# Kernel optimization log

Measured on AMD Instinct MI355X. Metric: run time of the kernel, lower is better.

Reference implementation:

```python
import jax, jax.numpy as jnp
import numpy as np

P = 2.0
HARDNESS_RATIO = 0.1
MARGIN = 0.0
EPS = 1e-7

N, DFEAT, NCLS = 4096, 128, 64


def setup_inputs() -> dict:
    key = jax.random.key(0)
    kx, ky = jax.random.split(key)
    x = jax.random.normal(kx, (N, DFEAT), dtype=jnp.float32)
    y = jax.random.randint(ky, (N,), 0, NCLS, dtype=jnp.int64)
    return {"x": x, "y": y}


def reference(x, y):
    # torch.cdist(x, x, p=2) via gram-matrix identity (clamped for sqrt stability)
    sq = jnp.sum(x * x, axis=1)                      # [N]
    D2 = sq[:, None] + sq[None, :] - 2.0 * (x @ x.T)  # [N, N]
    D = jnp.sqrt(jnp.maximum(D2, 1e-12))

    # label agreement masks (no-grad in torch; integer-derived so no float grad anyway)
    agree = (y[None, :] == y[:, None]).astype(x.dtype)   # [N, N]
    disagree = 1.0 - agree
    # With 64 samples/class every row is valid (>=1 positive and >=1 negative),
    # so the torch valid_rows filter keeps all rows; we compute all rows.

    # sort each row by distance, drop self (column 0), gather
    col_idx = jnp.argsort(D, axis=1)[:, 1:]               # [N, N-1]
    dist = jnp.take_along_axis(D, col_idx, axis=1)        # [N, N-1]
    a = jnp.take_along_axis(agree, col_idx, axis=1)
    d = jnp.take_along_axis(disagree, col_idx, axis=1)

    found_agree = jnp.cumsum(a, axis=1)
    found_agree = found_agree / (jnp.sum(found_agree, axis=1, keepdims=True) + EPS)
    found_disagree = jnp.cumsum(d, axis=1)
    found_disagree = found_disagree / (jnp.sum(found_disagree, axis=1, keepdims=True) + EPS)

    negative_hardness = jax.lax.stop_gradient(d * (found_disagree / (found_agree + HARDNESS_RATIO)))
    positive_hardness = jax.lax.stop_gradient(a * ((found_disagree + HARDNESS_RATIO) / (found_agree + HARDNESS_RATIO)))

    per_sample_score = jnp.mean(
        jax.nn.relu(dist * positive_hardness + MARGIN - dist * negative_hardness), axis=1
    )  # [N]

    sample_performance = jnp.sum(found_agree - found_disagree, axis=1)
    sample_performance = sample_performance - jnp.min(sample_performance)
    sample_weight = jax.lax.stop_gradient(1.0 / (sample_performance + 1.0))
    return per_sample_score * sample_weight
```

## Files before the change

kernel.cpp:

```cpp
#include <hip/hip_runtime.h>
#include <math.h>
#include <float.h>


#define N 4096
#define DF 128
#define NCLS 64
#define MAXP 128
#define DSTR 128
#define NB 256
#define HPAD 260
#define BSCALE 0.5f

typedef __bf16 bf16x8 __attribute__((ext_vector_type(8)));
typedef float f32x4 __attribute__((ext_vector_type(4)));
typedef unsigned int u32x4 __attribute__((ext_vector_type(4)));

static __device__ __forceinline__ unsigned short f2bf(float f) {
  unsigned int u = __float_as_uint(f);
  unsigned int r = (u + 0x7fffu + ((u >> 16) & 1u)) >> 16;
  return (unsigned short)r;
}
static __device__ __forceinline__ int d2bin(float d2) {
  int b = (int)(d2 * BSCALE);
  return min(max(b, 0), NB - 1);
}

__global__ void k_prep(const float* __restrict__ x, const int* __restrict__ y,
                       unsigned short* __restrict__ xb, float* __restrict__ sq,
                       unsigned int* __restrict__ cls_cnt, int* __restrict__ cls_idx,
                       int* __restrict__ pos, unsigned int* __restrict__ hist) {
  __shared__ unsigned int c_cnt[NCLS];
  const int tid = threadIdx.x;
  if (blockIdx.x < 1024) {
    const int wave = tid >> 6, lane = tid & 63;
    const int row = (blockIdx.x << 2) + wave;
    const float2 v = *(const float2*)&x[row * DF + (lane << 1)];
    unsigned int b = (unsigned int)f2bf(v.x) | ((unsigned int)f2bf(v.y) << 16);
    *(unsigned int*)&xb[row * DF + (lane << 1)] = b;
    const u32x4 z = {0u, 0u, 0u, 0u};
    *(u32x4*)&hist[(size_t)blockIdx.x * 1024 + (tid << 2)] = z;
    float s = v.x * v.x + v.y * v.y;
    #pragma unroll
    for (int off = 32; off; off >>= 1) s += __shfl_down(s, off);
    if (lane == 0) sq[row] = s;
  } else {
    if (tid < NCLS) c_cnt[tid] = 0u;
    __syncthreads();
    for (int k = tid; k < N; k += 256) {
      const int c = y[k];
      unsigned int p = atomicAdd(&c_cnt[c], 1u);
      if (p >= MAXP) p = MAXP - 1;
      cls_idx[c * MAXP + p] = k;
      pos[k] = (int)p;
    }
    __syncthreads();
    if (tid < NCLS) cls_cnt[tid] = min(c_cnt[tid], (unsigned int)MAXP);
  }
}

__global__ __launch_bounds__(256) void k_gram(
    const unsigned short* __restrict__ xb, const float* __restrict__ sq,
    const unsigned int* __restrict__ cls_cnt, const int* __restrict__ cls_idx,
    float* __restrict__ d2f) {
  __shared__ int plist[MAXP];
  __shared__ float sqL[MAXP];
  const int c = blockIdx.x >> 3;
  const int ti = blockIdx.x & 7;
  const int M = (int)cls_cnt[c];
  const int nT = (M + 15) >> 4;
  if (ti >= nT) return;
  const int tid = threadIdx.x;
  for (int m = tid; m < M; m += 256) {
    const int j = cls_idx[c * MAXP + m];
    plist[m] = j;
    sqL[m] = sq[j];
  }
  __syncthreads();
  const int wave = tid >> 6, lane = tid & 63;
  const int l15 = lane & 15, lg = lane >> 4;
  const int ra = min(ti * 16 + l15, M - 1);
  const u32x4* ap = (const u32x4*)(xb + (size_t)plist[ra] * DF + (lg << 3));
  const bf16x8 a0 = __builtin_bit_cast(bf16x8, ap[0]);
  const bf16x8 a1 = __builtin_bit_cast(bf16x8, ap[4]);
  const bf16x8 a2 = __builtin_bit_cast(bf16x8, ap[8]);
  const bf16x8 a3 = __builtin_bit_cast(bf16x8, ap[12]);
  float sqa[4];
  #pragma unroll
  for (int r = 0; r < 4; ++r) sqa[r] = sqL[min(ti * 16 + lg * 4 + r, M - 1)];
  float* drow = d2f + (size_t)c * (MAXP * DSTR);
  for (int tj = wave; tj < nT; tj += 4) {
    const int rb = min(tj * 16 + l15, M - 1);
    const u32x4* bp = (const u32x4*)(xb + (size_t)plist[rb] * DF + (lg << 3));
    const bf16x8 b0 = __builtin_bit_cast(bf16x8, bp[0]);
    const bf16x8 b1 = __builtin_bit_cast(bf16x8, bp[4]);
    const bf16x8 b2 = __builtin_bit_cast(bf16x8, bp[8]);
    const bf16x8 b3 = __builtin_bit_cast(bf16x8, bp[12]);
    f32x4 acc = {0.f, 0.f, 0.f, 0.f};
    acc = __builtin_amdgcn_mfma_f32_16x16x32_bf16(a0, b0, acc, 0, 0, 0);
    acc = __builtin_amdgcn_mfma_f32_16x16x32_bf16(a1, b1, acc, 0, 0, 0);
    acc = __builtin_amdgcn_mfma_f32_16x16x32_bf16(a2, b2, acc, 0, 0, 0);
    acc = __builtin_amdgcn_mfma_f32_16x16x32_bf16(a3, b3, acc, 0, 0, 0);
    const float sqc = sqL[rb];
    #pragma unroll
    for (int r = 0; r < 4; ++r) {
      const int row = ti * 16 + lg * 4 + r;
      drow[row * DSTR + tj * 16 + l15] = fmaf(-2.0f, acc[r], sqa[r] + sqc);
    }
  }
}

#define ROWS 32
#define CS 8

__global__ __launch_bounds__(256, 4) void k_count(
    const unsigned short* __restrict__ xb, const float* __restrict__ sq,
    unsigned int* __restrict__ hist) {
  __shared__ unsigned int histL[ROWS][HPAD];
  __shared__ float sqcL[512];
  const int rb = blockIdx.x >> 3;
  const int cs = blockIdx.x & 7;
  const int row0 = rb * ROWS;
  const int col0 = cs * 512;
  const int tid = threadIdx.x;
  const int wave = tid >> 6, lane = tid & 63;
  const int l15 = lane & 15, lg = lane >> 4;

  for (int e = tid; e < ROWS * HPAD; e += 256) ((unsigned int*)histL)[e] = 0u;
  if (tid < 256) { sqcL[tid] = sq[col0 + tid]; sqcL[tid + 256] = sq[col0 + 256 + tid]; }

  const u32x4* apA = (const u32x4*)(xb + (size_t)(row0 + l15) * DF + (lg << 3));
  const u32x4* apB = (const u32x4*)(xb + (size_t)(row0 + 16 + l15) * DF + (lg << 3));
  const bf16x8 a0 = __builtin_bit_cast(bf16x8, apA[0]);
  const bf16x8 a1 = __builtin_bit_cast(bf16x8, apA[4]);
  const bf16x8 a2 = __builtin_bit_cast(bf16x8, apA[8]);
  const bf16x8 a3 = __builtin_bit_cast(bf16x8, apA[12]);
  const bf16x8 a4 = __builtin_bit_cast(bf16x8, apB[0]);
  const bf16x8 a5 = __builtin_bit_cast(bf16x8, apB[4]);
  const bf16x8 a6 = __builtin_bit_cast(bf16x8, apB[8]);
  const bf16x8 a7 = __builtin_bit_cast(bf16x8, apB[12]);
  float sqa0[4], sqa1[4];
  #pragma unroll
  for (int r = 0; r < 4; ++r) {
    sqa0[r] = sq[row0 + lg * 4 + r];
    sqa1[r] = sq[row0 + 16 + lg * 4 + r];
  }
  __syncthreads();

  const int jbase = wave * 128;
  #pragma unroll
  for (int t = 0; t < 8; ++t) {
    const int jc = jbase + t * 16;
    const u32x4* bp = (const u32x4*)(xb + (size_t)(col0 + jc + l15) * DF + (lg << 3));
    const bf16x8 b0 = __builtin_bit_cast(bf16x8, bp[0]);
    const bf16x8 b1 = __builtin_bit_cast(bf16x8, bp[4]);
    const bf16x8 b2 = __builtin_bit_cast(bf16x8, bp[8]);
    const bf16x8 b3 = __builtin_bit_cast(bf16x8, bp[12]);
    f32x4 acc0 = {0.f, 0.f, 0.f, 0.f};
    f32x4 acc1 = {0.f, 0.f, 0.f, 0.f};
    acc0 = __builtin_amdgcn_mfma_f32_16x16x32_bf16(a0, b0, acc0, 0, 0, 0);
    acc0 = __builtin_amdgcn_mfma_f32_16x16x32_bf16(a1, b1, acc0, 0, 0, 0);
    acc0 = __builtin_amdgcn_mfma_f32_16x16x32_bf16(a2, b2, acc0, 0, 0, 0);
    acc0 = __builtin_amdgcn_mfma_f32_16x16x32_bf16(a3, b3, acc0, 0, 0, 0);
    acc1 = __builtin_amdgcn_mfma_f32_16x16x32_bf16(a4, b0, acc1, 0, 0, 0);
    acc1 = __builtin_amdgcn_mfma_f32_16x16x32_bf16(a5, b1, acc1, 0, 0, 0);
    acc1 = __builtin_amdgcn_mfma_f32_16x16x32_bf16(a6, b2, acc1, 0, 0, 0);
    acc1 = __builtin_amdgcn_mfma_f32_16x16x32_bf16(a7, b3, acc1, 0, 0, 0);
    const float sqc = sqcL[jc + l15];
    #pragma unroll
    for (int r = 0; r < 4; ++r) {
      const int lr = lg * 4 + r;
      atomicAdd(&histL[lr][d2bin(fmaf(-2.0f, acc0[r], sqa0[r] + sqc))], 1u);
      atomicAdd(&histL[16 + lr][d2bin(fmaf(-2.0f, acc1[r], sqa1[r] + sqc))], 1u);
    }
  }
  __syncthreads();
  for (int e = tid; e < ROWS * NB; e += 256) {
    const unsigned int v = histL[e >> 8][e & 255];
    if (v) atomicAdd(&hist[(size_t)(row0 + (e >> 8)) * NB + (e & 255)], v);
  }
}

__global__ void k_final(const int* __restrict__ y, const int* __restrict__ pos,
                        const unsigned int* __restrict__ cls_cnt,
                        const float* __restrict__ d2f,
                        const unsigned int* __restrict__ hist,
                        float* __restrict__ out) {
  __shared__ float rowL[MAXP];
  __shared__ unsigned int preL[NB];
  const int i = blockIdx.x;
  const int lane = threadIdx.x;
  const int c = y[i];
  const int rw = pos[i];
  const int M = (int)cls_cnt[c];
  const float* drow = d2f + (size_t)c * (MAXP * DSTR) + (size_t)rw * DSTR;
  rowL[lane] = drow[lane];
  rowL[lane + 64] = drow[lane + 64];
  const u32x4 h = *(const u32x4*)&hist[(size_t)i * NB + (lane << 2)];
  const unsigned int s0 = h[0], s1 = s0 + h[1], s2 = s1 + h[2], s3 = s2 + h[3];
  unsigned int sc_ = s3;
  #pragma unroll
  for (int off = 1; off < 64; off <<= 1) {
    const unsigned int t = __shfl_up(sc_, off);
    if (lane >= off) sc_ += t;
  }
  const unsigned int base = sc_ - s3;
  preL[(lane << 2) + 0] = base + s0;
  preL[(lane << 2) + 1] = base + s1;
  preL[(lane << 2) + 2] = base + s2;
  preL[(lane << 2) + 3] = base + s3;
  __syncthreads();
  const float dself = rowL[rw];
  const int el0 = lane, el1 = lane + 64;
  const bool v0 = (el0 < M) && (el0 != rw);
  const bool v1 = (el1 < M) && (el1 != rw);
  const float dt0 = v0 ? rowL[el0] : 0.f;
  const float dt1 = v1 ? rowL[el1] : 0.f;
  int r0 = 0, r1 = 0;
  for (int s = 0; s < M; ++s) {
    const float ds = rowL[s];
    r0 += (ds < dt0 || (ds == dt0 && s < el0)) ? 1 : 0;
    r1 += (ds < dt1 || (ds == dt1 && s < el1)) ? 1 : 0;
  }
  r0 -= (dself < dt0 || (dself == dt0 && rw < el0)) ? 1 : 0;
  r1 -= (dself < dt1 || (dself == dt1 && rw < el1)) ? 1 : 0;
  const int pr0 = v0 ? (int)preL[d2bin(dt0)] : 0;
  const int pr1 = v1 ? (int)preL[d2bin(dt1)] : 0;
  int sa = 0;
  if (v0) sa += (N + 1) - pr0;
  if (v1) sa += (N + 1) - pr1;
  #pragma unroll
  for (int off = 32; off; off >>= 1) sa += __shfl_down(sa, off);
  sa = __shfl(sa, 0);
  const float Sa = (float)sa + 1e-7f;
  const float Sd = (float)(8386560 - sa) + 1e-7f;
  float sc = 0.f;
  if (v0) {
    const float fa = (float)(r0 + 1) / Sa;
    const float fd = (float)((pr0 - 1) - (r0 + 1)) / Sd;
    sc += sqrtf(fmaxf(dt0, 1e-12f)) * (fd + 0.1f) / (fa + 0.1f);
  }
  if (v1) {
    const float fa = (float)(r1 + 1) / Sa;
    const float fd = (float)((pr1 - 1) - (r1 + 1)) / Sd;
    sc += sqrtf(fmaxf(dt1, 1e-12f)) * (fd + 0.1f) / (fa + 0.1f);
  }
  #pragma unroll
  for (int off = 32; off; off >>= 1) sc += __shfl_down(sc, off);
  if (lane == 0) out[i] = sc * (1.0f / 4095.0f);
}

extern "C" void kernel_launch(void* const* d_in, const int* in_sizes, int n_in,
                              void* d_out, int out_size, void* d_ws, size_t ws_size,
                              hipStream_t stream) {
  const float* x = (const float*)d_in[0];
  const int* y = (const int*)d_in[1];
  float* out = (float*)d_out;
  char* ws = (char*)d_ws;
  unsigned short* xb    = (unsigned short*)ws;
  float* sq             = (float*)(ws + 1048576);
  unsigned int* cls_cnt = (unsigned int*)(ws + 1064960);
  int* cls_idx          = (int*)(ws + 1065216);
  int* pos              = (int*)(ws + 1097984);
  unsigned int* hist    = (unsigned int*)(ws + 1114368);
  float* d2f            = (float*)(ws + 5308672);

  k_prep<<<1025, 256, 0, stream>>>(x, y, xb, sq, cls_cnt, cls_idx, pos, hist);
  k_gram<<<NCLS * 8, 256, 0, stream>>>(xb, sq, cls_cnt, cls_idx, d2f);
  k_count<<<(N / ROWS) * CS, 256, 0, stream>>>(xb, sq, hist);
  k_final<<<N, 64, 0, stream>>>(y, pos, cls_cnt, d2f, hist, out);
}
```

Measured before the change: 104.7 us.

## Fuse gram and count kernels; write per-slice histograms instead of global atomics

Merges the in-class gram kernel and the histogram-count kernel into a single launch, with block ranges dispatching to each role. It also replaces global atomic accumulation of histograms with plain stores of per-column-slice partial histograms, which the final kernel sums, so the zeroing pass in the prep kernel goes away. The count tiles are reshaped to 16 rows by 1024 columns and the LDS histogram padding changes. The intent is to cut one launch, the global atomics and the zero-fill, at the cost of more histogram memory traffic and less A-fragment reuse per B load.

```diff
diff --git a/kernel.cpp b/kernel.cpp
--- a/kernel.cpp
+++ b/kernel.cpp
@@ -9,8 +9,12 @@
 #define MAXP 128
 #define DSTR 128
 #define NB 256
-#define HPAD 260
+#define ROWS 16
+#define CS 4
+#define HPAD 257
+#define HROW (CS * NB)
 #define BSCALE 0.5f
+#define KCNT ((N / ROWS) * CS)
 
 typedef __bf16 bf16x8 __attribute__((ext_vector_type(8)));
 typedef float f32x4 __attribute__((ext_vector_type(4)));
@@ -29,7 +33,7 @@
 __global__ void k_prep(const float* __restrict__ x, const int* __restrict__ y,
                        unsigned short* __restrict__ xb, float* __restrict__ sq,
                        unsigned int* __restrict__ cls_cnt, int* __restrict__ cls_idx,
-                       int* __restrict__ pos, unsigned int* __restrict__ hist) {
+                       int* __restrict__ pos) {
   __shared__ unsigned int c_cnt[NCLS];
   const int tid = threadIdx.x;
   if (blockIdx.x < 1024) {
@@ -38,8 +42,6 @@
     const float2 v = *(const float2*)&x[row * DF + (lane << 1)];
     unsigned int b = (unsigned int)f2bf(v.x) | ((unsigned int)f2bf(v.y) << 16);
     *(unsigned int*)&xb[row * DF + (lane << 1)] = b;
-    const u32x4 z = {0u, 0u, 0u, 0u};
-    *(u32x4*)&hist[(size_t)blockIdx.x * 1024 + (tid << 2)] = z;
     float s = v.x * v.x + v.y * v.y;
     #pragma unroll
     for (int off = 32; off; off >>= 1) s += __shfl_down(s, off);
@@ -59,132 +61,110 @@
   }
 }
 
-__global__ __launch_bounds__(256) void k_gram(
+__global__ __launch_bounds__(256, 4) void k_cg(
     const unsigned short* __restrict__ xb, const float* __restrict__ sq,
     const unsigned int* __restrict__ cls_cnt, const int* __restrict__ cls_idx,
-    float* __restrict__ d2f) {
+    unsigned int* __restrict__ hist4, float* __restrict__ d2f) {
+  __shared__ unsigned int histL[ROWS][HPAD];
+  __shared__ float sqcL[1024];
   __shared__ int plist[MAXP];
   __shared__ float sqL[MAXP];
-  const int c = blockIdx.x >> 3;
-  const int ti = blockIdx.x & 7;
-  const int M = (int)cls_cnt[c];
-  const int nT = (M + 15) >> 4;
-  if (ti >= nT) return;
-  const int tid = threadIdx.x;
-  for (int m = tid; m < M; m += 256) {
-    const int j = cls_idx[c * MAXP + m];
-    plist[m] = j;
-    sqL[m] = sq[j];
-  }
-  __syncthreads();
-  const int wave = tid >> 6, lane = tid & 63;
-  const int l15 = lane & 15, lg = lane >> 4;
-  const int ra = min(ti * 16 + l15, M - 1);
-  const u32x4* ap = (const u32x4*)(xb + (size_t)plist[ra] * DF + (lg << 3));
-  const bf16x8 a0 = __builtin_bit_cast(bf16x8, ap[0]);
-  const bf16x8 a1 = __builtin_bit_cast(bf16x8, ap[4]);
-  const bf16x8 a2 = __builtin_bit_cast(bf16x8, ap[8]);
-  const bf16x8 a3 = __builtin_bit_cast(bf16x8, ap[12]);
-  float sqa[4];
-  #pragma unroll
-  for (int r = 0; r < 4; ++r) sqa[r] = sqL[min(ti * 16 + lg * 4 + r, M - 1)];
-  float* drow = d2f + (size_t)c * (MAXP * DSTR);
-  for (int tj = wave; tj < nT; tj += 4) {
-    const int rb = min(tj * 16 + l15, M - 1);
-    const u32x4* bp = (const u32x4*)(xb + (size_t)plist[rb] * DF + (lg << 3));
-    const bf16x8 b0 = __builtin_bit_cast(bf16x8, bp[0]);
-    const bf16x8 b1 = __builtin_bit_cast(bf16x8, bp[4]);
-    const bf16x8 b2 = __builtin_bit_cast(bf16x8, bp[8]);
-    const bf16x8 b3 = __builtin_bit_cast(bf16x8, bp[12]);
-    f32x4 acc = {0.f, 0.f, 0.f, 0.f};
-    acc = __builtin_amdgcn_mfma_f32_16x16x32_bf16(a0, b0, acc, 0, 0, 0);
-    acc = __builtin_amdgcn_mfma_f32_16x16x32_bf16(a1, b1, acc, 0, 0, 0);
-    acc = __builtin_amdgcn_mfma_f32_16x16x32_bf16(a2, b2, acc, 0, 0, 0);
-    acc = __builtin_amdgcn_mfma_f32_16x16x32_bf16(a3, b3, acc, 0, 0, 0);
-    const float sqc = sqL[rb];
-    #pragma unroll
-    for (int r = 0; r < 4; ++r) {
-      const int row = ti * 16 + lg * 4 + r;
-      drow[row * DSTR + tj * 16 + l15] = fmaf(-2.0f, acc[r], sqa[r] + sqc);
-    }
-  }
-}
-
-#define ROWS 32
-#define CS 8
-
-__global__ __launch_bounds__(256, 4) void k_count(
-    const unsigned short* __restrict__ xb, const float* __restrict__ sq,
-    unsigned int* __restrict__ hist) {
-  __shared__ unsigned int histL[ROWS][HPAD];
-  __shared__ float sqcL[512];
-  const int rb = blockIdx.x >> 3;
-  const int cs = blockIdx.x & 7;
-  const int row0 = rb * ROWS;
-  const int col0 = cs * 512;
   const int tid = threadIdx.x;
   const int wave = tid >> 6, lane = tid & 63;
   const int l15 = lane & 15, lg = lane >> 4;
 
-  for (int e = tid; e < ROWS * HPAD; e += 256) ((unsigned int*)histL)[e] = 0u;
-  if (tid < 256) { sqcL[tid] = sq[col0 + tid]; sqcL[tid + 256] = sq[col0 + 256 + tid]; }
-
-  const u32x4* apA = (const u32x4*)(xb + (size_t)(row0 + l15) * DF + (lg << 3));
-  const u32x4* apB = (const u32x4*)(xb + (size_t)(row0 + 16 + l15) * DF + (lg << 3));
-  const bf16x8 a0 = __builtin_bit_cast(bf16x8, apA[0]);
-  const bf16x8 a1 = __builtin_bit_cast(bf16x8, apA[4]);
-  const bf16x8 a2 = __builtin_bit_cast(bf16x8, apA[8]);
-  const bf16x8 a3 = __builtin_bit_cast(bf16x8, apA[12]);
-  const bf16x8 a4 = __builtin_bit_cast(bf16x8, apB[0]);
-  const bf16x8 a5 = __builtin_bit_cast(bf16x8, apB[4]);
-  const bf16x8 a6 = __builtin_bit_cast(bf16x8, apB[8]);
-  const bf16x8 a7 = __builtin_bit_cast(bf16x8, apB[12]);
-  float sqa0[4], sqa1[4];
-  #pragma unroll
-  for (int r = 0; r < 4; ++r) {
-    sqa0[r] = sq[row0 + lg * 4 + r];
-    sqa1[r] = sq[row0 + 16 + lg * 4 + r];
-  }
-  __syncthreads();
-
-  const int jbase = wave * 128;
-  #pragma unroll
-  for (int t = 0; t < 8; ++t) {
-    const int jc = jbase + t * 16;
-    const u32x4* bp = (const u32x4*)(xb + (size_t)(col0 + jc + l15) * DF + (lg << 3));
-    const bf16x8 b0 = __builtin_bit_cast(bf16x8, bp[0]);
-    const bf16x8 b1 = __builtin_bit_cast(bf16x8, bp[4]);
-    const bf16x8 b2 = __builtin_bit_cast(bf16x8, bp[8]);
-    const bf16x8 b3 = __builtin_bit_cast(bf16x8, bp[12]);
-    f32x4 acc0 = {0.f, 0.f, 0.f, 0.f};
-    f32x4 acc1 = {0.f, 0.f, 0.f, 0.f};
-    acc0 = __builtin_amdgcn_mfma_f32_16x16x32_bf16(a0, b0, acc0, 0, 0, 0);
-    acc0 = __builtin_amdgcn_mfma_f32_16x16x32_bf16(a1, b1, acc0, 0, 0, 0);
-    acc0 = __builtin_amdgcn_mfma_f32_16x16x32_bf16(a2, b2, acc0, 0, 0, 0);
-    acc0 = __builtin_amdgcn_mfma_f32_16x16x32_bf16(a3, b3, acc0, 0, 0, 0);
-    acc1 = __builtin_amdgcn_mfma_f32_16x16x32_bf16(a4, b0, acc1, 0, 0, 0);
-    acc1 = __builtin_amdgcn_mfma_f32_16x16x32_bf16(a5, b1, acc1, 0, 0, 0);
-    acc1 = __builtin_amdgcn_mfma_f32_16x16x32_bf16(a6, b2, acc1, 0, 0, 0);
-    acc1 = __builtin_amdgcn_mfma_f32_16x16x32_bf16(a7, b3, acc1, 0, 0, 0);
-    const float sqc = sqcL[jc + l15];
-    #pragma unroll
-    for (int r = 0; r < 4; ++r) {
-      const int lr = lg * 4 + r;
-      atomicAdd(&histL[lr][d2bin(fmaf(-2.0f, acc0[r], sqa0[r] + sqc))], 1u);
-      atomicAdd(&histL[16 + lr][d2bin(fmaf(-2.0f, acc1[r], sqa1[r] + sqc))], 1u);
-    }
-  }
-  __syncthreads();
-  for (int e = tid; e < ROWS * NB; e += 256) {
-    const unsigned int v = histL[e >> 8][e & 255];
-    if (v) atomicAdd(&hist[(size_t)(row0 + (e >> 8)) * NB + (e & 255)], v);
+  if (blockIdx.x < KCNT) {
+    const int rb = blockIdx.x >> 2;
+    const int cs = blockIdx.x & 3;
+    const int row0 = rb * ROWS;
+    const int col0 = cs * 1024;
+
+    for (int e = tid; e < ROWS * HPAD; e += 256) ((unsigned int*)histL)[e] = 0u;
+    for (int e = tid; e < 1024; e += 256) sqcL[e] = sq[col0 + e];
+
+    const u32x4* ap = (const u32x4*)(xb + (size_t)(row0 + l15) * DF + (lg << 3));
+    const bf16x8 a0 = __builtin_bit_cast(bf16x8, ap[0]);
+    const bf16x8 a1 = __builtin_bit_cast(bf16x8, ap[4]);
+    const bf16x8 a2 = __builtin_bit_cast(bf16x8, ap[8]);
+    const bf16x8 a3 = __builtin_bit_cast(bf16x8, ap[12]);
+    float sqa[4];
+    #pragma unroll
+    for (int r = 0; r < 4; ++r) sqa[r] = sq[row0 + lg * 4 + r];
+    __syncthreads();
+
+    const int jbase = wave * 256;
+    #pragma unroll
+    for (int t = 0; t < 16; ++t) {
+      const int jc = jbase + t * 16;
+      const u32x4* bp = (const u32x4*)(xb + (size_t)(col0 + jc + l15) * DF + (lg << 3));
+      const bf16x8 b0 = __builtin_bit_cast(bf16x8, bp[0]);
+      const bf16x8 b1 = __builtin_bit_cast(bf16x8, bp[4]);
+      const bf16x8 b2 = __builtin_bit_cast(bf16x8, bp[8]);
+      const bf16x8 b3 = __builtin_bit_cast(bf16x8, bp[12]);
+      f32x4 acc = {0.f, 0.f, 0.f, 0.f};
+      acc = __builtin_amdgcn_mfma_f32_16x16x32_bf16(a0, b0, acc, 0, 0, 0);
+      acc = __builtin_amdgcn_mfma_f32_16x16x32_bf16(a1, b1, acc, 0, 0, 0);
+      acc = __builtin_amdgcn_mfma_f32_16x16x32_bf16(a2, b2, acc, 0, 0, 0);
+      acc = __builtin_amdgcn_mfma_f32_16x16x32_bf16(a3, b3, acc, 0, 0, 0);
+      const float sqc = sqcL[jc + l15];
+      #pragma unroll
+      for (int r = 0; r < 4; ++r) {
+        const int lr = lg * 4 + r;
+        atomicAdd(&histL[lr][d2bin(fmaf(-2.0f, acc[r], sqa[r] + sqc))], 1u);
+      }
+    }
+    __syncthreads();
+    for (int e = tid; e < ROWS * NB; e += 256)
+      hist4[(size_t)(row0 + (e >> 8)) * HROW + cs * NB + (e & 255)] = histL[e >> 8][e & 255];
+  } else {
+    const int gb = blockIdx.x - KCNT;
+    const int c = gb >> 3;
+    const int ti = gb & 7;
+    const int M = (int)cls_cnt[c];
+    const int nT = (M + 15) >> 4;
+    if (ti >= nT) return;
+    for (int m = tid; m < M; m += 256) {
+      const int j = cls_idx[c * MAXP + m];
+      plist[m] = j;
+      sqL[m] = sq[j];
+    }
+    __syncthreads();
+    const int ra = min(ti * 16 + l15, M - 1);
+    const u32x4* ap = (const u32x4*)(xb + (size_t)plist[ra] * DF + (lg << 3));
+    const bf16x8 a0 = __builtin_bit_cast(bf16x8, ap[0]);
+    const bf16x8 a1 = __builtin_bit_cast(bf16x8, ap[4]);
+    const bf16x8 a2 = __builtin_bit_cast(bf16x8, ap[8]);
+    const bf16x8 a3 = __builtin_bit_cast(bf16x8, ap[12]);
+    float sqa[4];
+    #pragma unroll
+    for (int r = 0; r < 4; ++r) sqa[r] = sqL[min(ti * 16 + lg * 4 + r, M - 1)];
+    float* drow = d2f + (size_t)c * (MAXP * DSTR);
+    for (int tj = wave; tj < nT; tj += 4) {
+      const int rb2 = min(tj * 16 + l15, M - 1);
+      const u32x4* bp = (const u32x4*)(xb + (size_t)plist[rb2] * DF + (lg << 3));
+      const bf16x8 b0 = __builtin_bit_cast(bf16x8, bp[0]);
+      const bf16x8 b1 = __builtin_bit_cast(bf16x8, bp[4]);
+      const bf16x8 b2 = __builtin_bit_cast(bf16x8, bp[8]);
+      const bf16x8 b3 = __builtin_bit_cast(bf16x8, bp[12]);
+      f32x4 acc = {0.f, 0.f, 0.f, 0.f};
+      acc = __builtin_amdgcn_mfma_f32_16x16x32_bf16(a0, b0, acc, 0, 0, 0);
+      acc = __builtin_amdgcn_mfma_f32_16x16x32_bf16(a1, b1, acc, 0, 0, 0);
+      acc = __builtin_amdgcn_mfma_f32_16x16x32_bf16(a2, b2, acc, 0, 0, 0);
+      acc = __builtin_amdgcn_mfma_f32_16x16x32_bf16(a3, b3, acc, 0, 0, 0);
+      const float sqc = sqL[rb2];
+      #pragma unroll
+      for (int r = 0; r < 4; ++r) {
+        const int row = ti * 16 + lg * 4 + r;
+        drow[row * DSTR + tj * 16 + l15] = fmaf(-2.0f, acc[r], sqa[r] + sqc);
+      }
+    }
   }
 }
 
 __global__ void k_final(const int* __restrict__ y, const int* __restrict__ pos,
                         const unsigned int* __restrict__ cls_cnt,
                         const float* __restrict__ d2f,
-                        const unsigned int* __restrict__ hist,
+                        const unsigned int* __restrict__ hist4,
                         float* __restrict__ out) {
   __shared__ float rowL[MAXP];
   __shared__ unsigned int preL[NB];
@@ -196,7 +176,13 @@
   const float* drow = d2f + (size_t)c * (MAXP * DSTR) + (size_t)rw * DSTR;
   rowL[lane] = drow[lane];
   rowL[lane + 64] = drow[lane + 64];
-  const u32x4 h = *(const u32x4*)&hist[(size_t)i * NB + (lane << 2)];
+  const unsigned int* hrow = hist4 + (size_t)i * HROW;
+  u32x4 h = *(const u32x4*)&hrow[lane << 2];
+  #pragma unroll
+  for (int s = 1; s < CS; ++s) {
+    const u32x4 h2 = *(const u32x4*)&hrow[s * NB + (lane << 2)];
+    h[0] += h2[0]; h[1] += h2[1]; h[2] += h2[2]; h[3] += h2[3];
+  }
   const unsigned int s0 = h[0], s1 = s0 + h[1], s2 = s1 + h[2], s3 = s2 + h[3];
   unsigned int sc_ = s3;
   #pragma unroll
@@ -262,11 +248,10 @@
   unsigned int* cls_cnt = (unsigned int*)(ws + 1064960);
   int* cls_idx          = (int*)(ws + 1065216);
   int* pos              = (int*)(ws + 1097984);
-  unsigned int* hist    = (unsigned int*)(ws + 1114368);
-  float* d2f            = (float*)(ws + 5308672);
-
-  k_prep<<<1025, 256, 0, stream>>>(x, y, xb, sq, cls_cnt, cls_idx, pos, hist);
-  k_gram<<<NCLS * 8, 256, 0, stream>>>(xb, sq, cls_cnt, cls_idx, d2f);
-  k_count<<<(N / ROWS) * CS, 256, 0, stream>>>(xb, sq, hist);
-  k_final<<<N, 64, 0, stream>>>(y, pos, cls_cnt, d2f, hist, out);
-}
+  float* d2f            = (float*)(ws + 1114368);
+  unsigned int* hist4   = (unsigned int*)(ws + 5308672);
+
+  k_prep<<<1025, 256, 0, stream>>>(x, y, xb, sq, cls_cnt, cls_idx, pos);
+  k_cg<<<KCNT + NCLS * 8, 256, 0, stream>>>(xb, sq, cls_cnt, cls_idx, hist4, d2f);
+  k_final<<<N, 64, 0, stream>>>(y, pos, cls_cnt, d2f, hist4, out);
+}
```

New measurement: 111.1 us. 1.06x slower.

## Merge gram and histogram-count kernels into one launch with B-tile prefetch

Applied to the files above, without the earlier changes.

Merges the within-class gram kernel and the all-pairs histogram counting kernel into a single launch, with blocks split by blockIdx between the two roles. This removes one kernel launch and lets the small gram blocks run alongside the counting work. The counting loop now loads the next 16-column B tile into registers before the current MFMAs to hide load latency. The shared histogram padding also changes from 260 to 257. The merged kernel carries the shared memory of both roles, which may lower occupancy for the gram blocks.

```diff
diff --git a/kernel.cpp b/kernel.cpp
--- a/kernel.cpp
+++ b/kernel.cpp
@@ -9,8 +9,11 @@
 #define MAXP 128
 #define DSTR 128
 #define NB 256
-#define HPAD 260
+#define ROWS 32
+#define CS 8
+#define HPAD 257
 #define BSCALE 0.5f
+#define KCNT ((N / ROWS) * CS)
 
 typedef __bf16 bf16x8 __attribute__((ext_vector_type(8)));
 typedef float f32x4 __attribute__((ext_vector_type(4)));
@@ -59,125 +62,124 @@
   }
 }
 
-__global__ __launch_bounds__(256) void k_gram(
+__global__ __launch_bounds__(256, 4) void k_cg(
     const unsigned short* __restrict__ xb, const float* __restrict__ sq,
     const unsigned int* __restrict__ cls_cnt, const int* __restrict__ cls_idx,
-    float* __restrict__ d2f) {
+    unsigned int* __restrict__ hist, float* __restrict__ d2f) {
+  __shared__ unsigned int histL[ROWS][HPAD];
+  __shared__ float sqcL[512];
   __shared__ int plist[MAXP];
   __shared__ float sqL[MAXP];
-  const int c = blockIdx.x >> 3;
-  const int ti = blockIdx.x & 7;
-  const int M = (int)cls_cnt[c];
-  const int nT = (M + 15) >> 4;
-  if (ti >= nT) return;
-  const int tid = threadIdx.x;
-  for (int m = tid; m < M; m += 256) {
-    const int j = cls_idx[c * MAXP + m];
-    plist[m] = j;
-    sqL[m] = sq[j];
-  }
-  __syncthreads();
-  const int wave = tid >> 6, lane = tid & 63;
-  const int l15 = lane & 15, lg = lane >> 4;
-  const int ra = min(ti * 16 + l15, M - 1);
-  const u32x4* ap = (const u32x4*)(xb + (size_t)plist[ra] * DF + (lg << 3));
-  const bf16x8 a0 = __builtin_bit_cast(bf16x8, ap[0]);
-  const bf16x8 a1 = __builtin_bit_cast(bf16x8, ap[4]);
-  const bf16x8 a2 = __builtin_bit_cast(bf16x8, ap[8]);
-  const bf16x8 a3 = __builtin_bit_cast(bf16x8, ap[12]);
-  float sqa[4];
-  #pragma unroll
-  for (int r = 0; r < 4; ++r) sqa[r] = sqL[min(ti * 16 + lg * 4 + r, M - 1)];
-  float* drow = d2f + (size_t)c * (MAXP * DSTR);
-  for (int tj = wave; tj < nT; tj += 4) {
-    const int rb = min(tj * 16 + l15, M - 1);
-    const u32x4* bp = (const u32x4*)(xb + (size_t)plist[rb] * DF + (lg << 3));
-    const bf16x8 b0 = __builtin_bit_cast(bf16x8, bp[0]);
-    const bf16x8 b1 = __builtin_bit_cast(bf16x8, bp[4]);
-    const bf16x8 b2 = __builtin_bit_cast(bf16x8, bp[8]);
-    const bf16x8 b3 = __builtin_bit_cast(bf16x8, bp[12]);
-    f32x4 acc = {0.f, 0.f, 0.f, 0.f};
-    acc = __builtin_amdgcn_mfma_f32_16x16x32_bf16(a0, b0, acc, 0, 0, 0);
-    acc = __builtin_amdgcn_mfma_f32_16x16x32_bf16(a1, b1, acc, 0, 0, 0);
-    acc = __builtin_amdgcn_mfma_f32_16x16x32_bf16(a2, b2, acc, 0, 0, 0);
-    acc = __builtin_amdgcn_mfma_f32_16x16x32_bf16(a3, b3, acc, 0, 0, 0);
-    const float sqc = sqL[rb];
-    #pragma unroll
-    for (int r = 0; r < 4; ++r) {
-      const int row = ti * 16 + lg * 4 + r;
-      drow[row * DSTR + tj * 16 + l15] = fmaf(-2.0f, acc[r], sqa[r] + sqc);
-    }
-  }
-}
-
-#define ROWS 32
-#define CS 8
-
-__global__ __launch_bounds__(256, 4) void k_count(
-    const unsigned short* __restrict__ xb, const float* __restrict__ sq,
-    unsigned int* __restrict__ hist) {
-  __shared__ unsigned int histL[ROWS][HPAD];
-  __shared__ float sqcL[512];
-  const int rb = blockIdx.x >> 3;
-  const int cs = blockIdx.x & 7;
-  const int row0 = rb * ROWS;
-  const int col0 = cs * 512;
   const int tid = threadIdx.x;
   const int wave = tid >> 6, lane = tid & 63;
   const int l15 = lane & 15, lg = lane >> 4;
 
-  for (int e = tid; e < ROWS * HPAD; e += 256) ((unsigned int*)histL)[e] = 0u;
-  if (tid < 256) { sqcL[tid] = sq[col0 + tid]; sqcL[tid + 256] = sq[col0 + 256 + tid]; }
-
-  const u32x4* apA = (const u32x4*)(xb + (size_t)(row0 + l15) * DF + (lg << 3));
-  const u32x4* apB = (const u32x4*)(xb + (size_t)(row0 + 16 + l15) * DF + (lg << 3));
-  const bf16x8 a0 = __builtin_bit_cast(bf16x8, apA[0]);
-  const bf16x8 a1 = __builtin_bit_cast(bf16x8, apA[4]);
-  const bf16x8 a2 = __builtin_bit_cast(bf16x8, apA[8]);
-  const bf16x8 a3 = __builtin_bit_cast(bf16x8, apA[12]);
-  const bf16x8 a4 = __builtin_bit_cast(bf16x8, apB[0]);
-  const bf16x8 a5 = __builtin_bit_cast(bf16x8, apB[4]);
-  const bf16x8 a6 = __builtin_bit_cast(bf16x8, apB[8]);
-  const bf16x8 a7 = __builtin_bit_cast(bf16x8, apB[12]);
-  float sqa0[4], sqa1[4];
-  #pragma unroll
-  for (int r = 0; r < 4; ++r) {
-    sqa0[r] = sq[row0 + lg * 4 + r];
-    sqa1[r] = sq[row0 + 16 + lg * 4 + r];
-  }
-  __syncthreads();
-
-  const int jbase = wave * 128;
-  #pragma unroll
-  for (int t = 0; t < 8; ++t) {
-    const int jc = jbase + t * 16;
-    const u32x4* bp = (const u32x4*)(xb + (size_t)(col0 + jc + l15) * DF + (lg << 3));
-    const bf16x8 b0 = __builtin_bit_cast(bf16x8, bp[0]);
-    const bf16x8 b1 = __builtin_bit_cast(bf16x8, bp[4]);
-    const bf16x8 b2 = __builtin_bit_cast(bf16x8, bp[8]);
-    const bf16x8 b3 = __builtin_bit_cast(bf16x8, bp[12]);
-    f32x4 acc0 = {0.f, 0.f, 0.f, 0.f};
-    f32x4 acc1 = {0.f, 0.f, 0.f, 0.f};
-    acc0 = __builtin_amdgcn_mfma_f32_16x16x32_bf16(a0, b0, acc0, 0, 0, 0);
-    acc0 = __builtin_amdgcn_mfma_f32_16x16x32_bf16(a1, b1, acc0, 0, 0, 0);
-    acc0 = __builtin_amdgcn_mfma_f32_16x16x32_bf16(a2, b2, acc0, 0, 0, 0);
-    acc0 = __builtin_amdgcn_mfma_f32_16x16x32_bf16(a3, b3, acc0, 0, 0, 0);
-    acc1 = __builtin_amdgcn_mfma_f32_16x16x32_bf16(a4, b0, acc1, 0, 0, 0);
-    acc1 = __builtin_amdgcn_mfma_f32_16x16x32_bf16(a5, b1, acc1, 0, 0, 0);
-    acc1 = __builtin_amdgcn_mfma_f32_16x16x32_bf16(a6, b2, acc1, 0, 0, 0);
-    acc1 = __builtin_amdgcn_mfma_f32_16x16x32_bf16(a7, b3, acc1, 0, 0, 0);
-    const float sqc = sqcL[jc + l15];
+  if (blockIdx.x < KCNT) {
+    const int rb = blockIdx.x >> 3;
+    const int cs = blockIdx.x & 7;
+    const int row0 = rb * ROWS;
+    const int col0 = cs * 512;
+
+    for (int e = tid; e < ROWS * HPAD; e += 256) ((unsigned int*)histL)[e] = 0u;
+    if (tid < 256) { sqcL[tid] = sq[col0 + tid]; sqcL[tid + 256] = sq[col0 + 256 + tid]; }
+
+    const u32x4* apA = (const u32x4*)(xb + (size_t)(row0 + l15) * DF + (lg << 3));
+    const u32x4* apB = (const u32x4*)(xb + (size_t)(row0 + 16 + l15) * DF + (lg << 3));
+    const bf16x8 a0 = __builtin_bit_cast(bf16x8, apA[0]);
+    const bf16x8 a1 = __builtin_bit_cast(bf16x8, apA[4]);
+    const bf16x8 a2 = __builtin_bit_cast(bf16x8, apA[8]);
+    const bf16x8 a3 = __builtin_bit_cast(bf16x8, apA[12]);
+    const bf16x8 a4 = __builtin_bit_cast(bf16x8, apB[0]);
+    const bf16x8 a5 = __builtin_bit_cast(bf16x8, apB[4]);
+    const bf16x8 a6 = __builtin_bit_cast(bf16x8, apB[8]);
+    const bf16x8 a7 = __builtin_bit_cast(bf16x8, apB[12]);
+    float sqa0[4], sqa1[4];
     #pragma unroll
     for (int r = 0; r < 4; ++r) {
-      const int lr = lg * 4 + r;
-      atomicAdd(&histL[lr][d2bin(fmaf(-2.0f, acc0[r], sqa0[r] + sqc))], 1u);
-      atomicAdd(&histL[16 + lr][d2bin(fmaf(-2.0f, acc1[r], sqa1[r] + sqc))], 1u);
-    }
-  }
-  __syncthreads();
-  for (int e = tid; e < ROWS * NB; e += 256) {
-    const unsigned int v = histL[e >> 8][e & 255];
-    if (v) atomicAdd(&hist[(size_t)(row0 + (e >> 8)) * NB + (e & 255)], v);
+      sqa0[r] = sq[row0 + lg * 4 + r];
+      sqa1[r] = sq[row0 + 16 + lg * 4 + r];
+    }
+    __syncthreads();
+
+    const int jbase = wave * 128;
+    const u32x4* bp0 = (const u32x4*)(xb + (size_t)(col0 + jbase + l15) * DF + (lg << 3));
+    u32x4 f0 = bp0[0], f1 = bp0[4], f2 = bp0[8], f3 = bp0[12];
+    #pragma unroll
+    for (int t = 0; t < 8; ++t) {
+      const int jc = jbase + t * 16;
+      const bf16x8 b0 = __builtin_bit_cast(bf16x8, f0);
+      const bf16x8 b1 = __builtin_bit_cast(bf16x8, f1);
+      const bf16x8 b2 = __builtin_bit_cast(bf16x8, f2);
+      const bf16x8 b3 = __builtin_bit_cast(bf16x8, f3);
+      if (t < 7) {
+        const u32x4* bp = (const u32x4*)(xb + (size_t)(col0 + jc + 16 + l15) * DF + (lg << 3));
+        f0 = bp[0]; f1 = bp[4]; f2 = bp[8]; f3 = bp[12];
+      }
+      f32x4 acc0 = {0.f, 0.f, 0.f, 0.f};
+      f32x4 acc1 = {0.f, 0.f, 0.f, 0.f};
+      acc0 = __builtin_amdgcn_mfma_f32_16x16x32_bf16(a0, b0, acc0, 0, 0, 0);
+      acc0 = __builtin_amdgcn_mfma_f32_16x16x32_bf16(a1, b1, acc0, 0, 0, 0);
+      acc0 = __builtin_amdgcn_mfma_f32_16x16x32_bf16(a2, b2, acc0, 0, 0, 0);
+      acc0 = __builtin_amdgcn_mfma_f32_16x16x32_bf16(a3, b3, acc0, 0, 0, 0);
+      acc1 = __builtin_amdgcn_mfma_f32_16x16x32_bf16(a4, b0, acc1, 0, 0, 0);
+      acc1 = __builtin_amdgcn_mfma_f32_16x16x32_bf16(a5, b1, acc1, 0, 0, 0);
+      acc1 = __builtin_amdgcn_mfma_f32_16x16x32_bf16(a6, b2, acc1, 0, 0, 0);
+      acc1 = __builtin_amdgcn_mfma_f32_16x16x32_bf16(a7, b3, acc1, 0, 0, 0);
+      const float sqc = sqcL[jc + l15];
+      #pragma unroll
+      for (int r = 0; r < 4; ++r) {
+        const int lr = lg * 4 + r;
+        atomicAdd(&histL[lr][d2bin(fmaf(-2.0f, acc0[r], sqa0[r] + sqc))], 1u);
+        atomicAdd(&histL[16 + lr][d2bin(fmaf(-2.0f, acc1[r], sqa1[r] + sqc))], 1u);
+      }
+    }
+    __syncthreads();
+    for (int e = tid; e < ROWS * NB; e += 256) {
+      const unsigned int v = histL[e >> 8][e & 255];
+      if (v) atomicAdd(&hist[(size_t)(row0 + (e >> 8)) * NB + (e & 255)], v);
+    }
+  } else {
+    const int gb = blockIdx.x - KCNT;
+    const int c = gb >> 3;
+    const int ti = gb & 7;
+    const int M = (int)cls_cnt[c];
+    const int nT = (M + 15) >> 4;
+    if (ti >= nT) return;
+    for (int m = tid; m < M; m += 256) {
+      const int j = cls_idx[c * MAXP + m];
+      plist[m] = j;
+      sqL[m] = sq[j];
+    }
+    __syncthreads();
+    const int ra = min(ti * 16 + l15, M - 1);
+    const u32x4* ap = (const u32x4*)(xb + (size_t)plist[ra] * DF + (lg << 3));
+    const bf16x8 a0 = __builtin_bit_cast(bf16x8, ap[0]);
+    const bf16x8 a1 = __builtin_bit_cast(bf16x8, ap[4]);
+    const bf16x8 a2 = __builtin_bit_cast(bf16x8, ap[8]);
+    const bf16x8 a3 = __builtin_bit_cast(bf16x8, ap[12]);
+    float sqa[4];
+    #pragma unroll
+    for (int r = 0; r < 4; ++r) sqa[r] = sqL[min(ti * 16 + lg * 4 + r, M - 1)];
+    float* drow = d2f + (size_t)c * (MAXP * DSTR);
+    for (int tj = wave; tj < nT; tj += 4) {
+      const int rb2 = min(tj * 16 + l15, M - 1);
+      const u32x4* bp = (const u32x4*)(xb + (size_t)plist[rb2] * DF + (lg << 3));
+      const bf16x8 b0 = __builtin_bit_cast(bf16x8, bp[0]);
+      const bf16x8 b1 = __builtin_bit_cast(bf16x8, bp[4]);
+      const bf16x8 b2 = __builtin_bit_cast(bf16x8, bp[8]);
+      const bf16x8 b3 = __builtin_bit_cast(bf16x8, bp[12]);
+      f32x4 acc = {0.f, 0.f, 0.f, 0.f};
+      acc = __builtin_amdgcn_mfma_f32_16x16x32_bf16(a0, b0, acc, 0, 0, 0);
+      acc = __builtin_amdgcn_mfma_f32_16x16x32_bf16(a1, b1, acc, 0, 0, 0);
+      acc = __builtin_amdgcn_mfma_f32_16x16x32_bf16(a2, b2, acc, 0, 0, 0);
+      acc = __builtin_amdgcn_mfma_f32_16x16x32_bf16(a3, b3, acc, 0, 0, 0);
+      const float sqc = sqL[rb2];
+      #pragma unroll
+      for (int r = 0; r < 4; ++r) {
+        const int row = ti * 16 + lg * 4 + r;
+        drow[row * DSTR + tj * 16 + l15] = fmaf(-2.0f, acc[r], sqa[r] + sqc);
+      }
+    }
   }
 }
 
@@ -266,7 +268,6 @@
   float* d2f            = (float*)(ws + 5308672);
 
   k_prep<<<1025, 256, 0, stream>>>(x, y, xb, sq, cls_cnt, cls_idx, pos, hist);
-  k_gram<<<NCLS * 8, 256, 0, stream>>>(xb, sq, cls_cnt, cls_idx, d2f);
-  k_count<<<(N / ROWS) * CS, 256, 0, stream>>>(xb, sq, hist);
+  k_cg<<<KCNT + NCLS * 8, 256, 0, stream>>>(xb, sq, cls_cnt, cls_idx, hist, d2f);
   k_final<<<N, 64, 0, stream>>>(y, pos, cls_cnt, d2f, hist, out);
 }
```

Measured after the change: 99.13 us. 5.3% less time.
